# Kernel tuning notes

Hardware: AMD Instinct MI355X
Metric: run time of the kernel (lower is better)

Reference implementation:

```python
import jax, jax.numpy as jnp
import numpy as np

IMAGE_MAX_DIM = 1024
POOL = 7
NUM_CLASSES = 81
N_ROIS = 2000
BN_EPS = 1e-3


def _make_boxes(key, n):
    k1, k2, k3, k4 = jax.random.split(key, 4)
    cx = jax.random.uniform(k1, (n,), minval=0.0, maxval=IMAGE_MAX_DIM)
    cy = jax.random.uniform(k2, (n,), minval=0.0, maxval=IMAGE_MAX_DIM)
    w = jax.random.uniform(k3, (n,), minval=16.0, maxval=512.0)
    h = jax.random.uniform(k4, (n,), minval=16.0, maxval=512.0)
    x1 = jnp.clip(cx - w / 2, 0.0, IMAGE_MAX_DIM - 2.0)
    y1 = jnp.clip(cy - h / 2, 0.0, IMAGE_MAX_DIM - 2.0)
    x2 = jnp.clip(cx + w / 2, x1 + 1.0, IMAGE_MAX_DIM)
    y2 = jnp.clip(cy + h / 2, y1 + 1.0, IMAGE_MAX_DIM)
    return jnp.stack([x1, y1, x2, y2], axis=-1)[None]  # [1, n, 4]


def setup_inputs() -> dict:
    key = jax.random.key(0)
    ks = jax.random.split(key, 16)
    d = {
        'p2': jax.random.normal(ks[0], (1, 256, 256, 256), jnp.float32),
        'p3': jax.random.normal(ks[1], (1, 256, 128, 128), jnp.float32),
        'p4': jax.random.normal(ks[2], (1, 256, 64, 64), jnp.float32),
        'p5': jax.random.normal(ks[3], (1, 256, 32, 32), jnp.float32),
        'rpn_rois': _make_boxes(ks[4], N_ROIS),
        'conv1_w': jax.random.normal(ks[5], (1024, 256, POOL, POOL), jnp.float32) * 0.02,
        'conv1_b': jnp.zeros((1024,), jnp.float32),
        'bn1_g': jnp.ones((1024,), jnp.float32),
        'bn1_b': jnp.zeros((1024,), jnp.float32),
        'bn1_m': jnp.zeros((1024,), jnp.float32),
        'bn1_v': jnp.ones((1024,), jnp.float32),
        'conv2_w': jax.random.normal(ks[6], (1024, 1024), jnp.float32) * 0.02,
        'conv2_b': jnp.zeros((1024,), jnp.float32),
        'bn2_g': jnp.ones((1024,), jnp.float32),
        'bn2_b': jnp.zeros((1024,), jnp.float32),
        'bn2_m': jnp.zeros((1024,), jnp.float32),
        'bn2_v': jnp.ones((1024,), jnp.float32),
        'logits_w': jax.random.normal(ks[7], (NUM_CLASSES, 1024), jnp.float32) * 0.02,
        'logits_b': jnp.zeros((NUM_CLASSES,), jnp.float32),
        'bbox_w': jax.random.normal(ks[8], (NUM_CLASSES * 4, 1024), jnp.float32) * 0.02,
        'bbox_b': jnp.zeros((NUM_CLASSES * 4,), jnp.float32),
    }
    return d


def _crop_resize(fmap, boxes):
    """TF-style crop_and_resize, bilinear. fmap [C,H,W]; boxes [N,4] = (y1,x1,y2,x2) normalized."""
    C, H, W = fmap.shape
    dt = fmap.dtype
    y1, x1, y2, x2 = boxes[:, 0], boxes[:, 1], boxes[:, 2], boxes[:, 3]
    t = (jnp.arange(POOL, dtype=dt) / (POOL - 1))  # [P]
    ys = y1[:, None] * (H - 1) + t[None, :] * ((y2 - y1) * (H - 1))[:, None]  # [N,P]
    xs = x1[:, None] * (W - 1) + t[None, :] * ((x2 - x1) * (W - 1))[:, None]  # [N,P]
    y0 = jnp.floor(ys)
    x0 = jnp.floor(xs)
    ly = (ys - y0)[None, :, :, None]  # [1,N,P,1]
    lx = (xs - x0)[None, :, None, :]  # [1,N,1,P]
    y0i = jnp.clip(y0.astype(jnp.int32), 0, H - 1)
    y1i = jnp.clip(y0i + 1, 0, H - 1)
    x0i = jnp.clip(x0.astype(jnp.int32), 0, W - 1)
    x1i = jnp.clip(x0i + 1, 0, W - 1)

    def g(yi, xi):  # -> [C,N,P,P]
        return fmap[:, yi[:, :, None], xi[:, None, :]]

    out = (g(y0i, x0i) * (1 - ly) * (1 - lx) + g(y0i, x1i) * (1 - ly) * lx
           + g(y1i, x0i) * ly * (1 - lx) + g(y1i, x1i) * ly * lx)
    return jnp.transpose(out, (1, 0, 2, 3))  # [N,C,P,P]


def _forward(p2, p3, p4, p5, rpn_rois, conv1_w, conv1_b, bn1_g, bn1_b, bn1_m, bn1_v,
             conv2_w, conv2_b, bn2_g, bn2_b, bn2_m, bn2_v, logits_w, logits_b, bbox_w, bbox_b):
    rois = rpn_rois.reshape(-1, 4)  # [N,4] (x1,y1,x2,y2) in pixels
    x1, y1, x2, y2 = rois[:, 0], rois[:, 1], rois[:, 2], rois[:, 3]
    # level = clamp(round(log2(sqrt(area)/224)) + 4, 2, 5)
    roi_level = jnp.clip(jnp.round(jnp.log2(jnp.sqrt((y2 - y1) * (x2 - x1)) / 224.0)) + 4.0, 2.0, 5.0)
    boxes_n = (rois / float(IMAGE_MAX_DIM))[:, [1, 0, 3, 2]]  # (y1,x1,y2,x2) normalized

    pooled = jnp.zeros((rois.shape[0], 256, POOL, POOL), rois.dtype)
    for lvl, fmap in zip(range(2, 6), [p2, p3, p4, p5]):
        crops = _crop_resize(fmap[0], boxes_n)  # [N,256,P,P]
        mask = (roi_level == float(lvl))[:, None, None, None]
        pooled = pooled + jnp.where(mask, crops, 0.0)

    # conv1: 7x7 valid conv over [N,256,7,7] -> [N,1024]
    h = jnp.einsum('nchw,ochw->no', pooled, conv1_w) + conv1_b
    h = (h - bn1_m) * jax.lax.rsqrt(bn1_v + BN_EPS) * bn1_g + bn1_b
    h = jax.nn.relu(h)
    # conv2: 1x1 conv == matmul
    h = h @ conv2_w.T + conv2_b
    h = (h - bn2_m) * jax.lax.rsqrt(bn2_v + BN_EPS) * bn2_g + bn2_b
    shared = jax.nn.relu(h)  # [N,1024]

    logits = shared @ logits_w.T + logits_b
    probs = jax.nn.softmax(logits, axis=-1)
    bbox = shared @ bbox_w.T + bbox_b
    return (logits.reshape(1, N_ROIS, NUM_CLASSES),
            probs.reshape(1, N_ROIS, NUM_CLASSES),
            bbox.reshape(1, N_ROIS, NUM_CLASSES, 4))


def reference(p2, p3, p4, p5, rpn_rois, conv1_w, conv1_b, bn1_g, bn1_b, bn1_m, bn1_v,
              conv2_w, conv2_b, bn2_g, bn2_b, bn2_m, bn2_v, logits_w, logits_b, bbox_w, bbox_b):
    return _forward(p2, p3, p4, p5, rpn_rois, conv1_w, conv1_b, bn1_g, bn1_b, bn1_m, bn1_v,
                    conv2_w, conv2_b, bn2_g, bn2_b, bn2_m, bn2_v, logits_w, logits_b, bbox_w, bbox_b)
```

## Files before the change

### kernel.cpp

```cpp
#include <hip/hip_runtime.h>
#include <stdint.h>

#define NROI 2000
#define MPAD 2048
#define KP   12544
#define N1   1024
#define NCLS 81
#define NBOX 324
#define N3   405
#define N3P  448
#define BN_EPS 0.001f
#define KSPLIT 8

typedef __attribute__((ext_vector_type(8))) short bf16x8;
typedef __attribute__((ext_vector_type(4))) float f32x4;

__device__ inline unsigned short f2bf(float f) {
  union { float f; unsigned u; } v; v.f = f;
  unsigned r = v.u + 0x7fffu + ((v.u >> 16) & 1u);
  return (unsigned short)(r >> 16);
}

__device__ inline float bf2f(unsigned short h) {
  union { unsigned u; float f; } v; v.u = (unsigned)h << 16; return v.f;
}

__device__ inline void gld16(const unsigned short* g, unsigned short* l) {
  __builtin_amdgcn_global_load_lds(
      (const __attribute__((address_space(1))) void*)g,
      (__attribute__((address_space(3))) void*)l, 16, 0, 0);
}

__device__ __forceinline__ void kslice(int kz, int& off, int& len) {
  if (kz < 4) { off = kz * 1536; len = 1536; }
  else        { off = 6144 + (kz - 4) * 1600; len = 1600; }
}

__global__ __launch_bounds__(256) void front(
    const float* __restrict__ c1w, const float* __restrict__ c2w,
    const float* __restrict__ lw, const float* __restrict__ bw,
    const float* c1b, const float* g1, const float* b1, const float* m1, const float* v1,
    const float* c2b, const float* g2, const float* b2, const float* m2, const float* v2,
    const float* lb, const float* bb,
    const float* __restrict__ p2, const float* __restrict__ p3,
    const float* __restrict__ p4, const float* __restrict__ p5,
    unsigned short* __restrict__ w1p, unsigned short* __restrict__ w2b,
    unsigned short* __restrict__ w3b,
    unsigned short* __restrict__ f2t, unsigned short* __restrict__ f3t,
    unsigned short* __restrict__ f4t, unsigned short* __restrict__ f5t,
    float* s1, float* t1, float* s2, float* t2, float* b3) {
  __shared__ char smem_raw[64 * 260 * 2];
  int b = blockIdx.x;
  int t = threadIdx.x;
  if (b < 1024) {
    unsigned short* s = (unsigned short*)smem_raw;
    const float* src = c1w + (size_t)b * KP;
    for (int j = t; j < KP; j += 256) s[j] = f2bf(src[j]);
    __syncthreads();
    unsigned short* dst = w1p + (size_t)b * KP;
    int lane = t & 63, w = t >> 6;
    int c4 = lane * 4;
    for (int j = w; j < 49; j += 4) {
      ushort4 o;
      o.x = s[(c4 + 0) * 49 + j];
      o.y = s[(c4 + 1) * 49 + j];
      o.z = s[(c4 + 2) * 49 + j];
      o.w = s[(c4 + 3) * 49 + j];
      *(ushort4*)(dst + j * 256 + c4) = o;
    }
  } else if (b < 5120) {
    int j = (b - 1024) * 256 + t;
    w2b[j] = f2bf(c2w[j]);
  } else if (b < 5568) {
    int row = b - 5120;
    for (int k = t; k < 1024; k += 256) {
      float v = (row < NCLS) ? lw[row * 1024 + k]
                             : (row < N3 ? bw[(row - NCLS) * 1024 + k] : 0.0f);
      w3b[row * 1024 + k] = f2bf(v);
    }
  } else if (b == 5568) {
    for (int i = t; i < 1024; i += 256) {
      float sc = g1[i] * rsqrtf(v1[i] + BN_EPS);
      s1[i] = sc;
      t1[i] = (c1b[i] - m1[i]) * sc + b1[i];
      float ss = g2[i] * rsqrtf(v2[i] + BN_EPS);
      s2[i] = ss;
      t2[i] = (c2b[i] - m2[i]) * ss + b2[i];
    }
    for (int i = t; i < N3P; i += 256)
      b3[i] = (i < NCLS) ? lb[i] : (i < N3 ? bb[i - NCLS] : 0.0f);
  } else {
    typedef unsigned short lds_t[64][260];
    lds_t& s = *(lds_t*)smem_raw;
    int bb2 = b - 5569;
    const float* src;
    unsigned short* dst;
    int HW;
    if (bb2 < 1024)      { src = p2; dst = f2t; HW = 65536; }
    else if (bb2 < 1280) { bb2 -= 1024; src = p3; dst = f3t; HW = 16384; }
    else if (bb2 < 1344) { bb2 -= 1280; src = p4; dst = f4t; HW = 4096; }
    else                 { bb2 -= 1344; src = p5; dst = f5t; HW = 1024; }
    int p0 = bb2 * 64;
    int lane = t & 63, w = t >> 6;
    int px0 = (lane & 15) * 4;
#pragma unroll 4
    for (int it = 0; it < 16; ++it) {
      int c = w * 64 + it * 4 + (lane >> 4);
      float4 v = *(const float4*)(src + (size_t)c * HW + p0 + px0);
      s[px0 + 0][c] = f2bf(v.x);
      s[px0 + 1][c] = f2bf(v.y);
      s[px0 + 2][c] = f2bf(v.z);
      s[px0 + 3][c] = f2bf(v.w);
    }
    __syncthreads();
    int c4 = lane * 4;
#pragma unroll 4
    for (int i = 0; i < 16; ++i) {
      int p = w * 16 + i;
      ushort4 o = *(const ushort4*)&s[p][c4];
      *(ushort4*)(dst + (size_t)(p0 + p) * 256 + c4) = o;
    }
  }
}

__global__ __launch_bounds__(256) void roi_align2(
    const unsigned short* __restrict__ f2t, const unsigned short* __restrict__ f3t,
    const unsigned short* __restrict__ f4t, const unsigned short* __restrict__ f5t,
    const float* __restrict__ rois, unsigned short* __restrict__ pooled) {
  int n = blockIdx.x;
  int t = threadIdx.x;
  int lane = t & 63, w = t >> 6;
  int c0 = lane * 4;
  unsigned short* out = pooled + (size_t)n * KP;
  if (n >= NROI) {
    for (int p = w; p < 49; p += 4)
      *(ushort4*)(out + p * 256 + c0) = make_ushort4(0, 0, 0, 0);
    return;
  }
  float x1 = rois[n * 4 + 0], y1 = rois[n * 4 + 1];
  float x2 = rois[n * 4 + 2], y2 = rois[n * 4 + 3];
  float area = (y2 - y1) * (x2 - x1);
  float lvl_f = rintf(log2f(sqrtf(area) / 224.0f)) + 4.0f;
  lvl_f = fminf(fmaxf(lvl_f, 2.0f), 5.0f);
  int lvl = (int)lvl_f;
  const unsigned short* f;
  int H;
  if (lvl == 2)      { f = f2t; H = 256; }
  else if (lvl == 3) { f = f3t; H = 128; }
  else if (lvl == 4) { f = f4t; H = 64;  }
  else               { f = f5t; H = 32;  }
  int W = H;
  const float inv = 1.0f / 1024.0f;
  float yn1 = y1 * inv, xn1 = x1 * inv, yn2 = y2 * inv, xn2 = x2 * inv;
  float hs = (yn2 - yn1) * (H - 1);
  float ws = (xn2 - xn1) * (W - 1);
  float yb = yn1 * (H - 1);
  float xb = xn1 * (W - 1);

  for (int p = w; p < 49; p += 4) {
    int py = p / 7, px = p - py * 7;
    float ysv = yb + ((float)py / 6.0f) * hs;
    float xsv = xb + ((float)px / 6.0f) * ws;
    float y0f = floorf(ysv), x0f = floorf(xsv);
    float ly = ysv - y0f, lx = xsv - x0f;
    int y0 = min(max((int)y0f, 0), H - 1);
    int y1i = min(y0 + 1, H - 1);
    int x0 = min(max((int)x0f, 0), W - 1);
    int x1i = min(x0 + 1, W - 1);
    ushort4 v00 = *(const ushort4*)(f + ((size_t)y0 * W + x0) * 256 + c0);
    ushort4 v01 = *(const ushort4*)(f + ((size_t)y0 * W + x1i) * 256 + c0);
    ushort4 v10 = *(const ushort4*)(f + ((size_t)y1i * W + x0) * 256 + c0);
    ushort4 v11 = *(const ushort4*)(f + ((size_t)y1i * W + x1i) * 256 + c0);
    ushort4 o;
    {
      float a = bf2f(v00.x), bq = bf2f(v01.x), cq = bf2f(v10.x), d = bf2f(v11.x);
      float top = a + lx * (bq - a), bot = cq + lx * (d - cq);
      o.x = f2bf(top + ly * (bot - top));
    }
    {
      float a = bf2f(v00.y), bq = bf2f(v01.y), cq = bf2f(v10.y), d = bf2f(v11.y);
      float top = a + lx * (bq - a), bot = cq + lx * (d - cq);
      o.y = f2bf(top + ly * (bot - top));
    }
    {
      float a = bf2f(v00.z), bq = bf2f(v01.z), cq = bf2f(v10.z), d = bf2f(v11.z);
      float top = a + lx * (bq - a), bot = cq + lx * (d - cq);
      o.z = f2bf(top + ly * (bot - top));
    }
    {
      float a = bf2f(v00.w), bq = bf2f(v01.w), cq = bf2f(v10.w), d = bf2f(v11.w);
      float top = a + lx * (bq - a), bot = cq + lx * (d - cq);
      o.w = f2bf(top + ly * (bot - top));
    }
    *(ushort4*)(out + p * 256 + c0) = o;
  }
}

__global__ __launch_bounds__(256) void gemm1_sk(
    const unsigned short* __restrict__ A, const unsigned short* __restrict__ B,
    unsigned short* __restrict__ part) {
  __shared__ unsigned short As[128 * 64];
  __shared__ unsigned short Bs[128 * 64];
  int bid = blockIdx.x;
  int kz = bid & 7;
  int u = bid >> 3;
  int bn0 = (u & 7) * 128;
  int bm0 = (u >> 3) * 128;
  int koff, klen;
  kslice(kz, koff, klen);
  int t = threadIdx.x;
  int lane = t & 63, w = t >> 6;
  int wm = (w & 1) * 64, wn = (w >> 1) * 64;
  int ln = lane & 15, q = lane >> 4;

  int r8 = t >> 3, j8 = t & 7;
  int sj = j8 ^ (r8 & 7);
  const unsigned short* ga = A + (size_t)(bm0 + r8) * KP + koff + sj * 8;
  const unsigned short* gb = B + (size_t)(bn0 + r8) * KP + koff + sj * 8;
  unsigned short* la = &As[t * 8];
  unsigned short* lb = &Bs[t * 8];
  int e = ln & 7;

  f32x4 acc[4][4] = {};

  for (int k0 = 0; k0 < klen; k0 += 64) {
#pragma unroll
    for (int i = 0; i < 4; ++i) {
      gld16(ga + k0 + (size_t)(i * 32) * KP, la + i * 2048);
      gld16(gb + k0 + (size_t)(i * 32) * KP, lb + i * 2048);
    }
    __syncthreads();
#pragma unroll
    for (int h = 0; h < 2; ++h) {
      int slot = ((h * 4 + q) ^ e) * 8;
      bf16x8 af[4], bfr[4];
#pragma unroll
      for (int i = 0; i < 4; ++i) {
        af[i]  = *(const bf16x8*)&As[(wm + i * 16 + ln) * 64 + slot];
        bfr[i] = *(const bf16x8*)&Bs[(wn + i * 16 + ln) * 64 + slot];
      }
#pragma unroll
      for (int i = 0; i < 4; ++i)
#pragma unroll
        for (int j = 0; j < 4; ++j)
          acc[i][j] = __builtin_amdgcn_mfma_f32_16x16x32_bf16(af[i], bfr[j], acc[i][j], 0, 0, 0);
    }
    __syncthreads();
  }

  unsigned short* po = part + (size_t)kz * MPAD * N1;
#pragma unroll
  for (int i = 0; i < 4; ++i)
#pragma unroll
    for (int j = 0; j < 4; ++j)
#pragma unroll
      for (int r = 0; r < 4; ++r) {
        int m = bm0 + wm + i * 16 + q * 4 + r;
        int n = bn0 + wn + j * 16 + ln;
        po[(size_t)m * N1 + n] = f2bf(acc[i][j][r]);
      }
}

__global__ void reduce_sk(const unsigned short* __restrict__ part,
                          const float* __restrict__ sc, const float* __restrict__ sh,
                          unsigned short* __restrict__ outb) {
  const size_t P = (size_t)MPAD * N1;
  int m = blockIdx.x;
  int t = threadIdx.x;
  float4 v = {0.f, 0.f, 0.f, 0.f};
#pragma unroll
  for (int kz = 0; kz < KSPLIT; ++kz) {
    ushort4 u = *(const ushort4*)(part + kz * P + (size_t)m * N1 + t * 4);
    v.x += bf2f(u.x); v.y += bf2f(u.y); v.z += bf2f(u.z); v.w += bf2f(u.w);
  }
  int n0 = t * 4;
  ushort4 o;
  if (m < NROI) {
    o.x = f2bf(fmaxf(v.x * sc[n0 + 0] + sh[n0 + 0], 0.0f));
    o.y = f2bf(fmaxf(v.y * sc[n0 + 1] + sh[n0 + 1], 0.0f));
    o.z = f2bf(fmaxf(v.z * sc[n0 + 2] + sh[n0 + 2], 0.0f));
    o.w = f2bf(fmaxf(v.w * sc[n0 + 3] + sh[n0 + 3], 0.0f));
  } else {
    o = make_ushort4(0, 0, 0, 0);
  }
  *(ushort4*)(outb + (size_t)m * N1 + n0) = o;
}

template <int MODE>
__global__ __launch_bounds__(256) void gemm_bt(
    const unsigned short* __restrict__ A, const unsigned short* __restrict__ B,
    int M, int N, int K,
    const float* __restrict__ sc, const float* __restrict__ sh,
    unsigned short* __restrict__ outb, float* __restrict__ outf,
    int validM, int ldo) {
  __shared__ unsigned short As[64 * 64];
  __shared__ unsigned short Bs[64 * 64];
  int bm0 = blockIdx.y * 64;
  int bn0 = blockIdx.x * 64;
  int t = threadIdx.x;
  int lane = t & 63, w = t >> 6;
  int wm = (w & 1) * 32, wn = (w >> 1) * 32;
  int ln = lane & 15, q = lane >> 4;

  int r8 = t >> 3, j8 = t & 7;
  int sj = j8 ^ (r8 & 7);
  const unsigned short* ga = A + (size_t)(bm0 + r8) * K + sj * 8;
  const unsigned short* gb = B + (size_t)(bn0 + r8) * K + sj * 8;
  unsigned short* la = &As[t * 8];
  unsigned short* lb = &Bs[t * 8];
  int e = ln & 7;

  f32x4 acc00 = {0.f, 0.f, 0.f, 0.f}, acc01 = {0.f, 0.f, 0.f, 0.f};
  f32x4 acc10 = {0.f, 0.f, 0.f, 0.f}, acc11 = {0.f, 0.f, 0.f, 0.f};

  for (int k0 = 0; k0 < K; k0 += 64) {
    gld16(ga + k0, la);
    gld16(ga + k0 + (size_t)32 * K, la + 2048);
    gld16(gb + k0, lb);
    gld16(gb + k0 + (size_t)32 * K, lb + 2048);
    __syncthreads();
#pragma unroll
    for (int h = 0; h < 2; ++h) {
      int slot = ((h * 4 + q) ^ e) * 8;
      bf16x8 a0 = *(const bf16x8*)&As[(wm + ln) * 64 + slot];
      bf16x8 a1 = *(const bf16x8*)&As[(wm + 16 + ln) * 64 + slot];
      bf16x8 b0 = *(const bf16x8*)&Bs[(wn + ln) * 64 + slot];
      bf16x8 b1 = *(const bf16x8*)&Bs[(wn + 16 + ln) * 64 + slot];
      acc00 = __builtin_amdgcn_mfma_f32_16x16x32_bf16(a0, b0, acc00, 0, 0, 0);
      acc01 = __builtin_amdgcn_mfma_f32_16x16x32_bf16(a0, b1, acc01, 0, 0, 0);
      acc10 = __builtin_amdgcn_mfma_f32_16x16x32_bf16(a1, b0, acc10, 0, 0, 0);
      acc11 = __builtin_amdgcn_mfma_f32_16x16x32_bf16(a1, b1, acc11, 0, 0, 0);
    }
    __syncthreads();
  }

  f32x4 accs[2][2] = {{acc00, acc01}, {acc10, acc11}};
#pragma unroll
  for (int i = 0; i < 2; ++i)
#pragma unroll
    for (int j = 0; j < 2; ++j)
#pragma unroll
      for (int r = 0; r < 4; ++r) {
        int m = bm0 + wm + i * 16 + q * 4 + r;
        int n = bn0 + wn + j * 16 + ln;
        float v = accs[i][j][r];
        if (MODE == 1) {
          float o = fmaxf(v * sc[n] + sh[n], 0.0f);
          outb[(size_t)m * ldo + n] = (m < validM) ? f2bf(o) : (unsigned short)0;
        } else {
          outf[(size_t)m * ldo + n] = v + sh[n];
        }
      }
}

__global__ void head(const float* __restrict__ fc3, float* __restrict__ out) {
  int r = blockIdx.x;
  int t = threadIdx.x;
  const float* row = fc3 + (size_t)r * N3P;
  float v0 = (t < NCLS) ? row[t] : -INFINITY;
  float v1 = (t + 64 < NCLS) ? row[t + 64] : -INFINITY;
  float m = fmaxf(v0, v1);
#pragma unroll
  for (int o = 32; o > 0; o >>= 1) m = fmaxf(m, __shfl_xor(m, o, 64));
  float e0 = (t < NCLS) ? expf(v0 - m) : 0.0f;
  float e1 = (t + 64 < NCLS) ? expf(v1 - m) : 0.0f;
  float s = e0 + e1;
#pragma unroll
  for (int o = 32; o > 0; o >>= 1) s += __shfl_xor(s, o, 64);
  float invs = 1.0f / s;
  float* ol = out + (size_t)r * NCLS;
  float* op = out + 162000 + (size_t)r * NCLS;
  float* ob = out + 324000 + (size_t)r * NBOX;
  if (t < NCLS) { ol[t] = v0; op[t] = e0 * invs; }
  if (t + 64 < NCLS) { ol[t + 64] = v1; op[t + 64] = e1 * invs; }
  for (int j = t; j < NBOX; j += 64) ob[j] = row[NCLS + j];
}

extern "C" void kernel_launch(void* const* d_in, const int* in_sizes, int n_in,
                              void* d_out, int out_size, void* d_ws, size_t ws_size,
                              hipStream_t stream) {
  const float* p2  = (const float*)d_in[0];
  const float* p3  = (const float*)d_in[1];
  const float* p4  = (const float*)d_in[2];
  const float* p5  = (const float*)d_in[3];
  const float* roi = (const float*)d_in[4];
  const float* c1w = (const float*)d_in[5];
  const float* c1b = (const float*)d_in[6];
  const float* g1  = (const float*)d_in[7];
  const float* b1  = (const float*)d_in[8];
  const float* m1  = (const float*)d_in[9];
  const float* v1  = (const float*)d_in[10];
  const float* c2w = (const float*)d_in[11];
  const float* c2b = (const float*)d_in[12];
  const float* g2  = (const float*)d_in[13];
  const float* b2  = (const float*)d_in[14];
  const float* m2  = (const float*)d_in[15];
  const float* v2  = (const float*)d_in[16];
  const float* lw  = (const float*)d_in[17];
  const float* lb  = (const float*)d_in[18];
  const float* bw  = (const float*)d_in[19];
  const float* bb  = (const float*)d_in[20];
  float* out = (float*)d_out;

  char* ws = (char*)d_ws;
  size_t off = 0;
  auto alloc = [&](size_t bytes) {
    void* p = ws + off;
    off = (off + bytes + 255) & ~(size_t)255;
    return p;
  };
  unsigned short* pooled = (unsigned short*)alloc((size_t)MPAD * KP * 2);
  unsigned short* w1p    = (unsigned short*)alloc((size_t)N1 * KP * 2);
  unsigned short* w2b    = (unsigned short*)alloc((size_t)N1 * N1 * 2);
  unsigned short* w3b    = (unsigned short*)alloc((size_t)N3P * N1 * 2);
  unsigned short* a2     = (unsigned short*)alloc((size_t)MPAD * N1 * 2);
  unsigned short* shd    = (unsigned short*)alloc((size_t)MPAD * N1 * 2);
  float* fc3 = (float*)alloc((size_t)MPAD * N3P * 4);
  char* ub = (char*)alloc((size_t)48 * 1024 * 1024);
  unsigned short* f2t = (unsigned short*)ub;
  unsigned short* f3t = (unsigned short*)(ub + 33554432);
  unsigned short* f4t = (unsigned short*)(ub + 33554432 + 8388608);
  unsigned short* f5t = (unsigned short*)(ub + 33554432 + 8388608 + 2097152);
  unsigned short* part = (unsigned short*)ub;
  float* s1  = (float*)alloc(1024 * 4);
  float* t1  = (float*)alloc(1024 * 4);
  float* s2  = (float*)alloc(1024 * 4);
  float* t2  = (float*)alloc(1024 * 4);
  float* b3  = (float*)alloc(N3P * 4);

  front<<<6929, 256, 0, stream>>>(c1w, c2w, lw, bw,
                                  c1b, g1, b1, m1, v1, c2b, g2, b2, m2, v2,
                                  lb, bb, p2, p3, p4, p5,
                                  w1p, w2b, w3b, f2t, f3t, f4t, f5t,
                                  s1, t1, s2, t2, b3);

  roi_align2<<<MPAD, 256, 0, stream>>>(f2t, f3t, f4t, f5t, roi, pooled);

  gemm1_sk<<<1024, 256, 0, stream>>>(pooled, w1p, part);
  reduce_sk<<<MPAD, 256, 0, stream>>>(part, s1, t1, a2);

  gemm_bt<1><<<dim3(N1 / 64, MPAD / 64), 256, 0, stream>>>(
      a2, w2b, MPAD, N1, N1, s2, t2, shd, nullptr, NROI, N1);
  gemm_bt<2><<<dim3(N3P / 64, MPAD / 64), 256, 0, stream>>>(
      shd, w3b, MPAD, N3P, N1, nullptr, b3, nullptr, fc3, NROI, N3P);

  head<<<NROI, 64, 0, stream>>>(fc3, out);
}
```

Before: 338.2 us.

## Rewrite split-K conv1 GEMM with 256x256 tiles and double-buffered LDS pipeline

The split-K GEMM for conv1 now uses 512-thread blocks computing 256x256 output tiles instead of 128x128. Each wave holds an 8x4 MFMA accumulator tile. Global-to-LDS loads for the next K step are issued into a second buffer before the current step's MFMAs run, with explicit vmcnt waits, barriers and setprio around the compute. The aim is more operand reuse and hiding of global load latency. The cost is a launch of only 256 blocks, heavy register and LDS use (128 KB of shared memory), and less parallelism, which could cut occupancy on a GPU with many CUs.

```diff
diff --git a/kernel.cpp b/kernel.cpp
--- a/kernel.cpp
+++ b/kernel.cpp
@@ -196,69 +196,106 @@
   }
 }
 
-__global__ __launch_bounds__(256) void gemm1_sk(
+__global__ __launch_bounds__(512, 2) void gemm1_sk2(
     const unsigned short* __restrict__ A, const unsigned short* __restrict__ B,
     unsigned short* __restrict__ part) {
-  __shared__ unsigned short As[128 * 64];
-  __shared__ unsigned short Bs[128 * 64];
+  __shared__ unsigned short AsF[4 * 8192];
+  __shared__ unsigned short BsF[4 * 8192];
   int bid = blockIdx.x;
   int kz = bid & 7;
   int u = bid >> 3;
-  int bn0 = (u & 7) * 128;
-  int bm0 = (u >> 3) * 128;
+  int bn0 = (u & 3) * 256;
+  int bm0 = (u >> 2) * 256;
   int koff, klen;
   kslice(kz, koff, klen);
+  int nt = klen >> 6;
+
   int t = threadIdx.x;
   int lane = t & 63, w = t >> 6;
-  int wm = (w & 1) * 64, wn = (w >> 1) * 64;
+  int wr = w >> 2, wc = w & 3;
   int ln = lane & 15, q = lane >> 4;
 
-  int r8 = t >> 3, j8 = t & 7;
-  int sj = j8 ^ (r8 & 7);
-  const unsigned short* ga = A + (size_t)(bm0 + r8) * KP + koff + sj * 8;
-  const unsigned short* gb = B + (size_t)(bn0 + r8) * KP + koff + sj * 8;
-  unsigned short* la = &As[t * 8];
-  unsigned short* lb = &Bs[t * 8];
-  int e = ln & 7;
-
-  f32x4 acc[4][4] = {};
-
-  for (int k0 = 0; k0 < klen; k0 += 64) {
-#pragma unroll
-    for (int i = 0; i < 4; ++i) {
-      gld16(ga + k0 + (size_t)(i * 32) * KP, la + i * 2048);
-      gld16(gb + k0 + (size_t)(i * 32) * KP, lb + i * 2048);
-    }
-    __syncthreads();
-#pragma unroll
-    for (int h = 0; h < 2; ++h) {
-      int slot = ((h * 4 + q) ^ e) * 8;
-      bf16x8 af[4], bfr[4];
-#pragma unroll
-      for (int i = 0; i < 4; ++i) {
-        af[i]  = *(const bf16x8*)&As[(wm + i * 16 + ln) * 64 + slot];
-        bfr[i] = *(const bf16x8*)&Bs[(wn + i * 16 + ln) * 64 + slot];
-      }
-#pragma unroll
-      for (int i = 0; i < 4; ++i)
-#pragma unroll
-        for (int j = 0; j < 4; ++j)
-          acc[i][j] = __builtin_amdgcn_mfma_f32_16x16x32_bf16(af[i], bfr[j], acc[i][j], 0, 0, 0);
-    }
-    __syncthreads();
+  int clog = (lane & 3) ^ ((lane >> 3) & 3);
+  int l4 = lane >> 2;
+  const unsigned short* gA0 = A + (size_t)(bm0 + w * 32 + l4) * KP + koff + clog * 8;
+  const unsigned short* gA1 = gA0 + (size_t)16 * KP;
+  const unsigned short* gB0 = B + (size_t)(bn0 + w * 32 + l4) * KP + koff + clog * 8;
+  const unsigned short* gB1 = gB0 + (size_t)16 * KP;
+  int dc0 = (w * 128 + lane) * 8;
+  int dc1 = dc0 + 64 * 8;
+
+  int rxor = (q ^ ((ln >> 1) & 3)) * 8;
+  int rdA = (wr * 128 + ln) * 32 + rxor;
+  int rdB = (wc * 64 + ln) * 32 + rxor;
+
+  f32x4 acc[8][4] = {};
+
+#pragma unroll
+  for (int kk = 0; kk < 2; ++kk) {
+    int src = kk * 32;
+    int db = kk * 8192;
+    gld16(gA0 + src, AsF + db + dc0);
+    gld16(gA1 + src, AsF + db + dc1);
+    gld16(gB0 + src, BsF + db + dc0);
+    gld16(gB1 + src, BsF + db + dc1);
+  }
+  asm volatile("s_waitcnt vmcnt(4)" ::: "memory");
+  __builtin_amdgcn_s_barrier();
+  asm volatile("" ::: "memory");
+
+  for (int tt = 0; tt < nt; ++tt) {
+    int slot = tt & 1;
+    int nslot = slot ^ 1;
+    int knext = (tt + 1 < nt) ? (tt + 1) * 64 : 0;
+#pragma unroll
+    for (int kk = 0; kk < 2; ++kk) {
+      int rb = (slot * 2 + kk) * 8192;
+      bf16x8 af[8], bfr[4];
+#pragma unroll
+      for (int mi = 0; mi < 8; ++mi)
+        af[mi] = *(const bf16x8*)&AsF[rb + rdA + mi * 512];
+#pragma unroll
+      for (int nj = 0; nj < 4; ++nj)
+        bfr[nj] = *(const bf16x8*)&BsF[rb + rdB + nj * 512];
+
+      int src = knext + kk * 32;
+      int db = (nslot * 2 + kk) * 8192;
+      gld16(gA0 + src, AsF + db + dc0);
+      gld16(gA1 + src, AsF + db + dc1);
+      gld16(gB0 + src, BsF + db + dc0);
+      gld16(gB1 + src, BsF + db + dc1);
+
+      asm volatile("s_waitcnt vmcnt(4)" ::: "memory");
+      __builtin_amdgcn_s_barrier();
+      asm volatile("" ::: "memory");
+
+      __builtin_amdgcn_s_setprio(1);
+#pragma unroll
+      for (int mi = 0; mi < 8; ++mi)
+#pragma unroll
+        for (int nj = 0; nj < 4; ++nj)
+          acc[mi][nj] = __builtin_amdgcn_mfma_f32_16x16x32_bf16(
+              af[mi], bfr[nj], acc[mi][nj], 0, 0, 0);
+      __builtin_amdgcn_s_setprio(0);
+
+      asm volatile("" ::: "memory");
+      __builtin_amdgcn_s_barrier();
+      asm volatile("" ::: "memory");
+    }
   }
 
   unsigned short* po = part + (size_t)kz * MPAD * N1;
 #pragma unroll
-  for (int i = 0; i < 4; ++i)
-#pragma unroll
-    for (int j = 0; j < 4; ++j)
-#pragma unroll
-      for (int r = 0; r < 4; ++r) {
-        int m = bm0 + wm + i * 16 + q * 4 + r;
-        int n = bn0 + wn + j * 16 + ln;
-        po[(size_t)m * N1 + n] = f2bf(acc[i][j][r]);
-      }
+  for (int mi = 0; mi < 8; ++mi) {
+    int m = bm0 + wr * 128 + mi * 16 + q * 4;
+#pragma unroll
+    for (int nj = 0; nj < 4; ++nj) {
+      int n = bn0 + wc * 64 + nj * 16 + ln;
+#pragma unroll
+      for (int r = 0; r < 4; ++r)
+        po[(size_t)(m + r) * N1 + n] = f2bf(acc[mi][nj][r]);
+    }
+  }
 }
 
 __global__ void reduce_sk(const unsigned short* __restrict__ part,
@@ -436,7 +473,7 @@
 
   roi_align2<<<MPAD, 256, 0, stream>>>(f2t, f3t, f4t, f5t, roi, pooled);
 
-  gemm1_sk<<<1024, 256, 0, stream>>>(pooled, w1p, part);
+  gemm1_sk2<<<256, 512, 0, stream>>>(pooled, w1p, part);
   reduce_sk<<<MPAD, 256, 0, stream>>>(part, s1, t1, a2);
 
   gemm_bt<1><<<dim3(N1 / 64, MPAD / 64), 256, 0, stream>>>(
```

New measurement: 318.6 us. -5.8%, faster.
